# Kernel optimization log

Measured on AMD Instinct MI355X. Metric: run time of the kernel, lower is better.

## Reference

```python
import jax, jax.numpy as jnp
import numpy as np

D_MODEL, D_K, D_V = 128, 64, 64

def setup_inputs() -> dict:
    key = jax.random.key(0)
    ks = jax.random.split(key, 9)
    B, S = 4, 4096
    q_in = jax.random.normal(ks[0], (B, S, D_MODEL), dtype=jnp.float32)
    k_in = jax.random.normal(ks[1], (B, S, D_MODEL), dtype=jnp.float32)
    v_in = jax.random.normal(ks[2], (B, S, D_MODEL), dtype=jnp.float32)
    # glorot_uniform for kernels; original also uses glorot for biases
    def glorot(k, fan_in, fan_out, shape):
        lim = np.sqrt(6.0 / (fan_in + fan_out))
        return jax.random.uniform(k, shape, jnp.float32, -lim, lim)
    Wq = glorot(ks[3], D_MODEL, D_K, (D_MODEL, D_K)); bq = glorot(ks[4], D_MODEL, D_K, (D_K,))
    Wk = glorot(ks[5], D_MODEL, D_K, (D_MODEL, D_K)); bk = glorot(ks[6], D_MODEL, D_K, (D_K,))
    Wv = glorot(ks[7], D_MODEL, D_V, (D_MODEL, D_V)); bv = glorot(ks[8], D_MODEL, D_V, (D_V,))
    return {"q_in": q_in, "k_in": k_in, "v_in": v_in,
            "Wq": Wq, "bq": bq, "Wk": Wk, "bk": bk, "Wv": Wv, "bv": bv}

def reference(q_in, k_in, v_in, Wq, bq, Wk, bk, Wv, bv):
    q = q_in @ Wq + bq                      # [B,S,d_k]
    k = k_in @ Wk + bk                      # [B,S,d_k]
    v = v_in @ Wv + bv                      # [B,S,d_v]
    scores = jnp.einsum('bqd,bkd->bqk', q, k) / jnp.sqrt(jnp.float32(D_K))
    attn = jax.nn.softmax(scores, axis=-1)  # [B,S,S]
    return jnp.einsum('bqk,bkd->bqd', attn, v)
```

## Files before the change

### kernel.cpp

```cpp
#include <hip/hip_runtime.h>
#include <hip/hip_bf16.h>


using f32x4  = __attribute__((ext_vector_type(4)))  float;
using f32x16 = __attribute__((ext_vector_type(16))) float;
using s16x8  = __attribute__((ext_vector_type(8)))  short;

#define MFMA16(a, b, c) __builtin_amdgcn_mfma_f32_16x16x32_bf16((a), (b), (c), 0, 0, 0)
#define MFMA32(a, b, c) __builtin_amdgcn_mfma_f32_32x32x16_bf16((a), (b), (c), 0, 0, 0)

constexpr int SEQ = 4096;
constexpr int DM  = 128;
constexpr int DV  = 64;
constexpr int B_  = 4;
constexpr float LOG2E = 1.44269504f;
constexpr float SHIFT = 16.0f;

static __device__ __forceinline__ unsigned short f2bf(float f) {
  union { float f; unsigned u; } x; x.f = f;
  unsigned r = x.u + 0x7fffu + ((x.u >> 16) & 1u);
  return (unsigned short)(r >> 16);
}

static __device__ __forceinline__ unsigned cvt_pk_bf16(float lo, float hi) {
  unsigned d;
  asm("v_cvt_pk_bf16_f32 %0, %1, %2" : "=v"(d) : "v"(lo), "v"(hi));
  return d;
}

static __device__ __forceinline__ float bf2f(unsigned short h) {
  union { unsigned u; float f; } x; x.u = ((unsigned)h) << 16;
  return x.f;
}

static __device__ __forceinline__ float exp2_hw(float x) {
  float d;
  asm("v_exp_f32 %0, %1" : "=v"(d) : "v"(x));
  return d;
}

static __device__ __forceinline__ void gll16(const unsigned short* g,
                                             unsigned short* l) {
  __builtin_amdgcn_global_load_lds(
      (const __attribute__((address_space(1))) unsigned int*)g,
      (__attribute__((address_space(3))) unsigned int*)l, 16, 0, 0);
}

__global__ __launch_bounds__(256) void proj_kernel(
    const float* __restrict__ q_in, const float* __restrict__ k_in,
    const float* __restrict__ v_in,
    const float* __restrict__ Wq, const float* __restrict__ bq,
    const float* __restrict__ Wk, const float* __restrict__ bk,
    const float* __restrict__ Wv, const float* __restrict__ bv,
    unsigned short* __restrict__ qp, unsigned short* __restrict__ kp,
    unsigned short* __restrict__ vpT)
{
  __shared__ unsigned short Wt[64][136];
  const int tid = threadIdx.x;
  const int m = blockIdx.y;
  const float* W    = (m == 0) ? Wq : (m == 1) ? Wk : Wv;
  const float* in   = (m == 0) ? q_in : (m == 1) ? k_in : v_in;
  const float* bias = (m == 0) ? bq : (m == 1) ? bk : bv;

  for (int idx = tid; idx < DM * DV; idx += 256) {
    const int k = idx >> 6, c = idx & 63;
    Wt[c][k] = f2bf(W[idx]);
  }
  __syncthreads();

  const int w = tid >> 6, l = tid & 63;
  const int lr = l & 15, lg = l >> 4;
  const int rowbase = blockIdx.x * 64 + w * 16;

  f32x4 acc[4] = {};
  #pragma unroll
  for (int ks = 0; ks < 4; ++ks) {
    const float* ap = in + (size_t)(rowbase + lr) * DM + ks * 32 + lg * 8;
    const float4 a0 = *(const float4*)ap;
    const float4 a1 = *(const float4*)(ap + 4);
    s16x8 af;
    af[0] = (short)f2bf(a0.x); af[1] = (short)f2bf(a0.y);
    af[2] = (short)f2bf(a0.z); af[3] = (short)f2bf(a0.w);
    af[4] = (short)f2bf(a1.x); af[5] = (short)f2bf(a1.y);
    af[6] = (short)f2bf(a1.z); af[7] = (short)f2bf(a1.w);
    #pragma unroll
    for (int nt = 0; nt < 4; ++nt) {
      const s16x8 bfm = *(const s16x8*)&Wt[nt * 16 + lr][ks * 32 + lg * 8];
      acc[nt] = MFMA16(af, bfm, acc[nt]);
    }
  }
  const float scale = (m == 0) ? 0.125f : 1.0f;
  #pragma unroll
  for (int nt = 0; nt < 4; ++nt) {
    const int col = nt * 16 + lr;
    const float bb = bias[col];
    #pragma unroll
    for (int r = 0; r < 4; ++r) {
      const int row = rowbase + lg * 4 + r;
      const unsigned short val = f2bf((acc[nt][r] + bb) * scale);
      if (m == 0)      qp[(size_t)row * DV + col] = val;
      else if (m == 1) kp[(size_t)row * DV + col] = val;
      else             vpT[((size_t)(row >> 12) * DV + col) * SEQ + (row & (SEQ - 1))] = val;
    }
  }
}

static __device__ __forceinline__ s16x8 lds_read_sw(const unsigned short* base,
                                                    int row, int cb) {
  return *(const s16x8*)((const char*)base + row * 128 + (cb ^ ((row & 7) << 4)));
}

__global__ __launch_bounds__(256, 4) void attn_split_kernel(
    const unsigned short* __restrict__ qp, const unsigned short* __restrict__ kp,
    const unsigned short* __restrict__ vpT,
    unsigned short* __restrict__ OpartH, float* __restrict__ lpart,
    float* __restrict__ dout, int klen)
{
  __shared__ unsigned short Kl[2][64 * 64];
  __shared__ unsigned short Vt[2][64 * 64];

  const int tid = threadIdx.x, wq = tid >> 6, l = tid & 63;
  const int l31 = l & 31, hi = l >> 5;
  const int b = blockIdx.y, sp = blockIdx.z;
  const size_t boff = (size_t)b * SEQ * DV;
  const int qrow = blockIdx.x * 128 + wq * 32 + l31;
  const int kstart = sp * klen, kend = kstart + klen;

  s16x8 qf[4];
  {
    const unsigned short* qpr = qp + boff + (size_t)qrow * DV + 8 * hi;
    #pragma unroll
    for (int ks = 0; ks < 4; ++ks)
      qf[ks] = *(const s16x8*)(qpr + 16 * ks);
  }

  const int lrow8 = l >> 3;
  const int xsw   = (((l & 7) ^ (lrow8 & 7)) << 4) >> 1;
  const int c0 = 2 * wq, c1 = 2 * wq + 1;
  const unsigned short* kgb = kp + boff;
  const unsigned short* vgb = vpT + boff;

  #define STAGE_TILE(buf, kb_) do {                                          \
    const unsigned short* kR0 = kgb + (size_t)((kb_) + 8*c0 + lrow8) * DV + xsw; \
    const unsigned short* kR1 = kgb + (size_t)((kb_) + 8*c1 + lrow8) * DV + xsw; \
    gll16(kR0, &Kl[buf][c0 * 512]);                                          \
    gll16(kR1, &Kl[buf][c1 * 512]);                                          \
    const unsigned short* vR0 = vgb + (size_t)(8*c0 + lrow8) * SEQ + (kb_) + xsw; \
    const unsigned short* vR1 = vgb + (size_t)(8*c1 + lrow8) * SEQ + (kb_) + xsw; \
    gll16(vR0, &Vt[buf][c0 * 512]);                                          \
    gll16(vR1, &Vt[buf][c1 * 512]);                                          \
  } while (0)

  STAGE_TILE(0, kstart);
  __syncthreads();

  f32x16 oacc[2] = {};
  f32x4 lacc4 = {};
  int cur = 0;

  for (int kb = kstart; kb < kend; kb += 64) {
    const bool more = (kb + 64 < kend);
    if (more) STAGE_TILE(cur ^ 1, kb + 64);

    const unsigned short* Kc = Kl[cur];
    f32x16 sacc[2] = {};
    __builtin_amdgcn_s_setprio(1);
    #pragma unroll
    for (int ks = 0; ks < 4; ++ks) {
      const int cb = 32 * ks + 16 * hi;
      const s16x8 kf0 = lds_read_sw(Kc, l31, cb);
      const s16x8 kf1 = lds_read_sw(Kc, 32 + l31, cb);
      sacc[0] = MFMA32(kf0, qf[ks], sacc[0]);
      sacc[1] = MFMA32(kf1, qf[ks], sacc[1]);
    }
    __builtin_amdgcn_s_setprio(0);

    #pragma unroll
    for (int mt = 0; mt < 2; ++mt)
      #pragma unroll
      for (int i = 0; i < 16; ++i)
        sacc[mt][i] = exp2_hw(fmaf(sacc[mt][i], LOG2E, -SHIFT));

    const unsigned short* Vc = Vt[cur];
    __builtin_amdgcn_s_setprio(1);
    #pragma unroll
    for (int ki = 0; ki < 4; ++ki) {
      const int mt = ki >> 1, w8 = (ki & 1) * 8;
      unsigned a0 = cvt_pk_bf16(sacc[mt][w8 + 0], sacc[mt][w8 + 1]);
      unsigned a1 = cvt_pk_bf16(sacc[mt][w8 + 2], sacc[mt][w8 + 3]);
      unsigned b0 = cvt_pk_bf16(sacc[mt][w8 + 4], sacc[mt][w8 + 5]);
      unsigned b1 = cvt_pk_bf16(sacc[mt][w8 + 6], sacc[mt][w8 + 7]);
      asm("v_permlane32_swap_b32 %0, %1" : "+v"(a0), "+v"(b0));
      asm("v_permlane32_swap_b32 %0, %1" : "+v"(a1), "+v"(b1));
      union { unsigned u[4]; s16x8 v; } pf;
      pf.u[0] = a0; pf.u[1] = a1; pf.u[2] = b0; pf.u[3] = b1;
      const int cb = 32 * ki + 16 * hi;
      const s16x8 vf0 = lds_read_sw(Vc, l31, cb);
      const s16x8 vf1 = lds_read_sw(Vc, 32 + l31, cb);
      oacc[0] = MFMA32(vf0, pf.v, oacc[0]);
      oacc[1] = MFMA32(vf1, pf.v, oacc[1]);
    }
    __builtin_amdgcn_s_setprio(0);

    {
      float t8[8];
      #pragma unroll
      for (int i = 0; i < 8; ++i)
        t8[i] = (sacc[0][i] + sacc[0][i + 8]) + (sacc[1][i] + sacc[1][i + 8]);
      #pragma unroll
      for (int i = 0; i < 4; ++i) lacc4[i] += t8[i] + t8[i + 4];
    }

    __syncthreads();
    cur ^= 1;
  }
  #undef STAGE_TILE

  float lsum = (lacc4[0] + lacc4[1]) + (lacc4[2] + lacc4[3]);
  lsum += __shfl_xor(lsum, 32);
  const float rinv = 1.0f / lsum;

  if (dout) {
    float* op = dout + boff + (size_t)qrow * DV;
    #pragma unroll
    for (int mt = 0; mt < 2; ++mt)
      #pragma unroll
      for (int g = 0; g < 4; ++g) {
        const int d0 = 32 * mt + 8 * g + 4 * hi;
        float4 v4;
        v4.x = oacc[mt][4 * g + 0] * rinv; v4.y = oacc[mt][4 * g + 1] * rinv;
        v4.z = oacc[mt][4 * g + 2] * rinv; v4.w = oacc[mt][4 * g + 3] * rinv;
        *(float4*)(op + d0) = v4;
      }
  } else {
    const size_t po = ((size_t)sp * B_ + b) * SEQ * DV;
    unsigned short* op = OpartH + po + (size_t)qrow * DV;
    #pragma unroll
    for (int mt = 0; mt < 2; ++mt)
      #pragma unroll
      for (int g = 0; g < 4; ++g) {
        const int d0 = 32 * mt + 8 * g + 4 * hi;
        uint2 u2;
        u2.x = cvt_pk_bf16(oacc[mt][4 * g + 0] * rinv, oacc[mt][4 * g + 1] * rinv);
        u2.y = cvt_pk_bf16(oacc[mt][4 * g + 2] * rinv, oacc[mt][4 * g + 3] * rinv);
        *(uint2*)(op + d0) = u2;
      }
    if (l < 32) {
      const size_t mo = ((size_t)sp * B_ + b) * SEQ + blockIdx.x * 128 + wq * 32 + l;
      lpart[mo] = lsum;
    }
  }
}

__global__ __launch_bounds__(256) void combine_kernel(
    const unsigned short* __restrict__ OpartH, const float* __restrict__ lpart,
    float* __restrict__ out, int nsplit)
{
  const int g = blockIdx.x * 256 + threadIdx.x;
  const int row = g >> 3;
  const int c8 = g & 7;
  const size_t rstride = (size_t)B_ * SEQ;

  float denom = 0.0f;
  float o[8] = {};
  for (int sp = 0; sp < nsplit; ++sp) {
    const float wgt = lpart[sp * rstride + row];
    denom += wgt;
    const s16x8 h = *(const s16x8*)&OpartH[sp * rstride * DV + (size_t)row * DV + c8 * 8];
    #pragma unroll
    for (int j = 0; j < 8; ++j) o[j] += wgt * bf2f((unsigned short)h[j]);
  }
  const float inv = 1.0f / denom;
  float4 v0, v1;
  v0.x = o[0] * inv; v0.y = o[1] * inv; v0.z = o[2] * inv; v0.w = o[3] * inv;
  v1.x = o[4] * inv; v1.y = o[5] * inv; v1.z = o[6] * inv; v1.w = o[7] * inv;
  float* op = out + (size_t)row * DV + c8 * 8;
  *(float4*)op = v0;
  *(float4*)(op + 4) = v1;
}

extern "C" void kernel_launch(void* const* d_in, const int* in_sizes, int n_in,
                              void* d_out, int out_size, void* d_ws, size_t ws_size,
                              hipStream_t stream) {
  const float* q_in = (const float*)d_in[0];
  const float* k_in = (const float*)d_in[1];
  const float* v_in = (const float*)d_in[2];
  const float* Wq   = (const float*)d_in[3];
  const float* bq   = (const float*)d_in[4];
  const float* Wk   = (const float*)d_in[5];
  const float* bk   = (const float*)d_in[6];
  const float* Wv   = (const float*)d_in[7];
  const float* bv   = (const float*)d_in[8];

  const size_t nproj = (size_t)B_ * SEQ * DV;
  unsigned short* qp  = (unsigned short*)d_ws;
  unsigned short* kp  = qp + nproj;
  unsigned short* vpT = kp + nproj;
  char* after = (char*)(vpT + nproj);
  const size_t used_base = (size_t)((char*)after - (char*)d_ws);

  int nsplit = 8;
  while (nsplit > 1) {
    const size_t need = used_base + (size_t)nsplit * B_ * SEQ * (DV * 2 + 4);
    if (need <= ws_size) break;
    nsplit >>= 1;
  }
  const bool direct = (nsplit == 1) &&
      (used_base + (size_t)B_ * SEQ * (DV * 2 + 4) > ws_size);

  unsigned short* OpartH = (unsigned short*)after;
  float* lpart = (float*)(OpartH + (size_t)nsplit * B_ * SEQ * DV);
  float* out = (float*)d_out;

  proj_kernel<<<dim3(256, 3), dim3(256), 0, stream>>>(
      q_in, k_in, v_in, Wq, bq, Wk, bk, Wv, bv, qp, kp, vpT);

  attn_split_kernel<<<dim3(SEQ / 128, B_, nsplit), dim3(256), 0, stream>>>(
      qp, kp, vpT, direct ? nullptr : OpartH, lpart,
      direct ? out : nullptr, SEQ / nsplit);

  if (!direct) {
    combine_kernel<<<dim3(B_ * SEQ * DV / 8 / 256), dim3(256), 0, stream>>>(
        OpartH, lpart, out, nsplit);
  }
}
```

Before: 46.87 us.

## Triple-buffer K tiles and use partial vmcnt waits in attention loop

K tiles move to a three-stage LDS ring and are prefetched two iterations ahead, while V stays double-buffered and is prefetched one ahead. The full __syncthreads at the end of each iteration becomes a partial s_waitcnt vmcnt(2) plus a raw s_barrier, so the K loads two tiles ahead can stay in flight across the barrier. The aim is to hide more global-load latency behind the QK and PV MFMAs. The extra K buffer adds 8KB of LDS per block, which may limit occupancy under the 4-blocks-per-CU launch bound. The hand-counted vmcnt values must match the number of outstanding loads exactly.

```diff
diff --git a/kernel.cpp b/kernel.cpp
--- a/kernel.cpp
+++ b/kernel.cpp
@@ -116,7 +116,7 @@
     unsigned short* __restrict__ OpartH, float* __restrict__ lpart,
     float* __restrict__ dout, int klen)
 {
-  __shared__ unsigned short Kl[2][64 * 64];
+  __shared__ unsigned short Kl[3][64 * 64];
   __shared__ unsigned short Vt[2][64 * 64];
 
   const int tid = threadIdx.x, wq = tid >> 6, l = tid & 63;
@@ -124,7 +124,8 @@
   const int b = blockIdx.y, sp = blockIdx.z;
   const size_t boff = (size_t)b * SEQ * DV;
   const int qrow = blockIdx.x * 128 + wq * 32 + l31;
-  const int kstart = sp * klen, kend = kstart + klen;
+  const int kstart = sp * klen;
+  const int ntiles = klen / 64;
 
   s16x8 qf[4];
   {
@@ -140,29 +141,40 @@
   const unsigned short* kgb = kp + boff;
   const unsigned short* vgb = vpT + boff;
 
-  #define STAGE_TILE(buf, kb_) do {                                          \
-    const unsigned short* kR0 = kgb + (size_t)((kb_) + 8*c0 + lrow8) * DV + xsw; \
-    const unsigned short* kR1 = kgb + (size_t)((kb_) + 8*c1 + lrow8) * DV + xsw; \
-    gll16(kR0, &Kl[buf][c0 * 512]);                                          \
-    gll16(kR1, &Kl[buf][c1 * 512]);                                          \
-    const unsigned short* vR0 = vgb + (size_t)(8*c0 + lrow8) * SEQ + (kb_) + xsw; \
-    const unsigned short* vR1 = vgb + (size_t)(8*c1 + lrow8) * SEQ + (kb_) + xsw; \
-    gll16(vR0, &Vt[buf][c0 * 512]);                                          \
-    gll16(vR1, &Vt[buf][c1 * 512]);                                          \
+  #define STAGE_K(buf, kb_) do {                                             \
+    gll16(kgb + (size_t)((kb_) + 8*c0 + lrow8) * DV + xsw, &Kl[buf][c0*512]); \
+    gll16(kgb + (size_t)((kb_) + 8*c1 + lrow8) * DV + xsw, &Kl[buf][c1*512]); \
   } while (0)
-
-  STAGE_TILE(0, kstart);
-  __syncthreads();
+  #define STAGE_V(buf, kb_) do {                                             \
+    gll16(vgb + (size_t)(8*c0 + lrow8) * SEQ + (kb_) + xsw, &Vt[buf][c0*512]); \
+    gll16(vgb + (size_t)(8*c1 + lrow8) * SEQ + (kb_) + xsw, &Vt[buf][c1*512]); \
+  } while (0)
+
+  STAGE_K(0, kstart);
+  STAGE_V(0, kstart);
+  if (ntiles > 1) {
+    STAGE_K(1, kstart + 64);
+    asm volatile("s_waitcnt vmcnt(2)" ::: "memory");
+  } else {
+    asm volatile("s_waitcnt vmcnt(0)" ::: "memory");
+  }
+  __builtin_amdgcn_sched_barrier(0);
+  __builtin_amdgcn_s_barrier();
+  __builtin_amdgcn_sched_barrier(0);
 
   f32x16 oacc[2] = {};
   f32x4 lacc4 = {};
-  int cur = 0;
-
-  for (int kb = kstart; kb < kend; kb += 64) {
-    const bool more = (kb + 64 < kend);
-    if (more) STAGE_TILE(cur ^ 1, kb + 64);
-
-    const unsigned short* Kc = Kl[cur];
+  int ks0 = 0;
+
+  for (int t = 0; t < ntiles; ++t) {
+    const int kb = kstart + t * 64;
+    if (t + 1 < ntiles) STAGE_V((t + 1) & 1, kb + 64);
+    if (t + 2 < ntiles) {
+      int s2 = ks0 + 2; if (s2 >= 3) s2 -= 3;
+      STAGE_K(s2, kb + 128);
+    }
+
+    const unsigned short* Kc = Kl[ks0];
     f32x16 sacc[2] = {};
     __builtin_amdgcn_s_setprio(1);
     #pragma unroll
@@ -181,7 +193,7 @@
       for (int i = 0; i < 16; ++i)
         sacc[mt][i] = exp2_hw(fmaf(sacc[mt][i], LOG2E, -SHIFT));
 
-    const unsigned short* Vc = Vt[cur];
+    const unsigned short* Vc = Vt[t & 1];
     __builtin_amdgcn_s_setprio(1);
     #pragma unroll
     for (int ki = 0; ki < 4; ++ki) {
@@ -211,10 +223,17 @@
       for (int i = 0; i < 4; ++i) lacc4[i] += t8[i] + t8[i + 4];
     }
 
-    __syncthreads();
-    cur ^= 1;
-  }
-  #undef STAGE_TILE
+    if (t + 1 < ntiles) {
+      if (t + 2 < ntiles) { asm volatile("s_waitcnt vmcnt(2)" ::: "memory"); }
+      else                { asm volatile("s_waitcnt vmcnt(0)" ::: "memory"); }
+      __builtin_amdgcn_sched_barrier(0);
+      __builtin_amdgcn_s_barrier();
+      __builtin_amdgcn_sched_barrier(0);
+    }
+    ks0 = (ks0 + 1 == 3) ? 0 : ks0 + 1;
+  }
+  #undef STAGE_K
+  #undef STAGE_V
 
   float lsum = (lacc4[0] + lacc4[1]) + (lacc4[2] + lacc4[3]);
   lsum += __shfl_xor(lsum, 32);
```

Result: slower. 52.71 us (+12.5%).
